# Performance work log

Hardware: AMD Instinct MI355X
Metric: run time of the kernel (lower is better)

## Reference

```python
import jax, jax.numpy as jnp
import numpy as np

N, E, G = 10000, 160000, 64          # nodes, edges, graphs
T, FIN, ED, FOUT = 5, 75, 50, 15     # towers, channels, edge-emb dim, per-tower out
EPS_BN, EPS_STD = 1e-5, 1e-5


def setup_inputs() -> dict:
    key = jax.random.key(0)
    ks = jax.random.split(key, 16)
    s = 0.05
    return dict(
        x=jax.random.randint(ks[0], (N,), 0, 21),
        edge_index=jax.random.randint(ks[1], (2, E), 0, N),
        edge_attr=jax.random.randint(ks[2], (E,), 0, 4),
        batch=jnp.sort(jax.random.randint(ks[3], (N,), 0, G)),
        node_emb=jax.random.normal(ks[4], (21, FIN), dtype=jnp.float32),
        edge_emb=jax.random.normal(ks[5], (4, ED), dtype=jnp.float32),
        We=jax.random.normal(ks[6], (4, ED, FIN), dtype=jnp.float32) * s,
        be=jnp.zeros((4, FIN), jnp.float32),
        Wpre=jax.random.normal(ks[7], (4, T, 3 * FIN, FIN), dtype=jnp.float32) * s,
        bpre=jnp.zeros((4, T, FIN), jnp.float32),
        Wpost=jax.random.normal(ks[8], (4, T, 13 * FIN, FOUT), dtype=jnp.float32) * s,
        bpost=jnp.zeros((4, T, FOUT), jnp.float32),
        Wlin=jax.random.normal(ks[9], (4, FIN, FIN), dtype=jnp.float32) * s,
        blin=jnp.zeros((4, FIN), jnp.float32),
        bn_gamma=jnp.ones((4, FIN), jnp.float32),
        bn_beta=jnp.zeros((4, FIN), jnp.float32),
        uaf=jnp.array([1.1, -0.01, 1e-5, -0.9, 1e-5], dtype=jnp.float32),
        mW1=jax.random.normal(ks[10], (FIN, 50), dtype=jnp.float32) * s,
        mb1=jnp.zeros((50,), jnp.float32),
        mW2=jax.random.normal(ks[11], (50, 25), dtype=jnp.float32) * s,
        mb2=jnp.zeros((25,), jnp.float32),
        mW3=jax.random.normal(ks[12], (25, 1), dtype=jnp.float32) * s,
        mb3=jnp.zeros((1,), jnp.float32),
    )


def _uaf(v, p):
    # softplus(A*(x+B) + C*x^2) - softplus(D*(x-B)) + E
    return (jax.nn.softplus(p[0] * (v + p[1]) + p[2] * v * v)
            - jax.nn.softplus(p[3] * (v - p[1])) + p[4])


def _pna_layer(h, src, dst, e_feat, We, be, Wpre, bpre, Wpost, bpost, Wl, bl,
               deg, avg_log):
    eemb = e_feat @ We + be                      # [E, FIN] edge encoder
    x_i, x_j = h[dst], h[src]                    # [E, FIN] gathers
    # pre-MLP: per-tower Linear(cat[x_i, x_j, e], 3F -> F), split weight blocks
    W1, W2, W3 = Wpre[:, :FIN], Wpre[:, FIN:2 * FIN], Wpre[:, 2 * FIN:]
    m = (jnp.einsum('ec,tcf->etf', x_i, W1)
         + jnp.einsum('ec,tcf->etf', x_j, W2)
         + jnp.einsum('ec,tcf->etf', eemb, W3) + bpre)   # [E, T, FIN]
    degc = jnp.maximum(deg, 1.0)[:, None, None]
    mean = jax.ops.segment_sum(m, dst, N) / degc          # [N, T, FIN]
    mean_sq = jax.ops.segment_sum(m * m, dst, N) / degc
    empty = (deg == 0.0)[:, None, None]
    mn = jnp.where(empty, 0.0, jax.ops.segment_min(m, dst, N))
    mx = jnp.where(empty, 0.0, jax.ops.segment_max(m, dst, N))
    std = jnp.sqrt(jax.nn.relu(mean_sq - mean * mean) + EPS_STD)
    agg = jnp.concatenate([mean, mn, mx, std], axis=-1)   # [N, T, 4F]
    amp = (jnp.log(jnp.maximum(deg, 1.0) + 1.0) / avg_log)[:, None, None]
    out = jnp.concatenate([agg, agg * amp, agg / amp], axis=-1)  # [N, T, 12F]
    # cat tower input (divide_input=False -> full x per tower)
    out = jnp.concatenate(
        [jnp.broadcast_to(h[:, None, :], (N, T, FIN)), out], axis=-1)  # [N,T,13F]
    out = jnp.einsum('ntc,tcf->ntf', out, Wpost) + bpost  # [N, T, FOUT]
    return out.reshape(N, T * FOUT) @ Wl + bl             # [N, FIN]


def reference(node_emb, edge_emb, We, be, Wpre, bpre, Wpost, bpost, Wlin, blin,
              bn_gamma, bn_beta, uaf, mW1, mb1, mW2, mb2, mW3, mb3,
              x, edge_index, edge_attr, batch):
    src, dst = edge_index[0], edge_index[1]
    h = node_emb[x]                              # [N, 75]
    e_feat = edge_emb[edge_attr]                 # [E, 50]
    deg = jax.ops.segment_sum(jnp.ones((E,), h.dtype), dst, N)
    avg_log = jnp.mean(jnp.log(deg + 1.0))       # PNA avg degree (log) statistic
    for l in range(4):
        out = _pna_layer(h, src, dst, e_feat, We[l], be[l], Wpre[l], bpre[l],
                         Wpost[l], bpost[l], Wlin[l], blin[l], deg, avg_log)
        mu = out.mean(axis=0)
        var = out.var(axis=0)                    # biased, training-mode BN
        out = (out - mu) * jax.lax.rsqrt(var + EPS_BN) * bn_gamma[l] + bn_beta[l]
        h = _uaf(out, uaf)
    pooled = jax.ops.segment_sum(h, batch, G)    # global_add_pool -> [G, 75]
    z = _uaf(pooled @ mW1 + mb1, uaf)
    z = _uaf(z @ mW2 + mb2, uaf)
    return z @ mW3 + mb3                         # [G, 1]
```

## Files before the change

### kernel.cpp

```cpp
#include <hip/hip_runtime.h>
#include <hip/hip_fp16.h>
#include <math.h>

static constexpr int N_   = 10000;
static constexpr int E_   = 160000;
static constexpr int G_   = 64;
static constexpr int T_   = 5;
static constexpr int FIN_ = 75;
static constexpr int ED_  = 50;
static constexpr int FOUT_= 15;
static constexpr int TF_  = T_*FIN_;
static constexpr int AGGW_= 4*FIN_;
static constexpr int YC_  = 48;
static constexpr int NP_  = 10112;
static constexpr int AW_  = 400;
static constexpr int BW_  = 384;
static constexpr int WK_  = 380;

__device__ __forceinline__ float softplus_f(float x){
    return fmaxf(x, 0.f) + log1pf(expf(-fabsf(x)));
}
__device__ __forceinline__ float uaf_f(float v, const float* __restrict__ p){
    return softplus_f(p[0]*(v + p[1]) + p[2]*v*v) - softplus_f(p[3]*(v - p[1])) + p[4];
}
__device__ __forceinline__ unsigned pack2h(float a, float b){
    __half2 h = __floats2half2_rn(a, b);
    return *reinterpret_cast<unsigned*>(&h);
}

__global__ void k_h0(const int* __restrict__ x, const float* __restrict__ node_emb, float* __restrict__ hT){
    int i = blockIdx.x*blockDim.x + threadIdx.x;
    if (i >= 80*N_) return;
    int q = i / N_, n = i % N_;
    hT[(size_t)q*NP_ + n] = (q < FIN_) ? node_emb[x[n]*FIN_ + q] : 0.f;
}

__global__ void k_deg(const int* __restrict__ ei, int* __restrict__ deg_i){
    int e = blockIdx.x*blockDim.x + threadIdx.x;
    if (e >= E_) return;
    atomicAdd(&deg_i[ei[E_ + e]], 1);
}

__global__ void k_scan(const int* __restrict__ deg_i, int* __restrict__ offs, float* __restrict__ avglog){
    __shared__ int sd[1024];
    __shared__ float sf[1024];
    __shared__ int carry;
    if (threadIdx.x == 0) carry = 0;
    __syncthreads();
    float ls = 0.f;
    for (int base = 0; base < N_; base += 1024){
        int i = base + threadIdx.x;
        int v = (i < N_) ? deg_i[i] : 0;
        if (i < N_) ls += logf((float)v + 1.f);
        sd[threadIdx.x] = v;
        __syncthreads();
        for (int off = 1; off < 1024; off <<= 1){
            int t = (threadIdx.x >= off) ? sd[threadIdx.x - off] : 0;
            __syncthreads();
            sd[threadIdx.x] += t;
            __syncthreads();
        }
        if (i < N_) offs[i] = carry + sd[threadIdx.x] - v;
        __syncthreads();
        if (threadIdx.x == 0) carry += sd[1023];
        __syncthreads();
    }
    if (threadIdx.x == 0) offs[N_] = carry;
    sf[threadIdx.x] = ls;
    __syncthreads();
    for (int off = 512; off > 0; off >>= 1){
        if (threadIdx.x < off) sf[threadIdx.x] += sf[threadIdx.x + off];
        __syncthreads();
    }
    if (threadIdx.x == 0) avglog[0] = sf[0] / (float)N_;
}

__global__ void k_fill(const int* __restrict__ ei, const int* __restrict__ eattr,
                       const int* __restrict__ offs, int* __restrict__ cursor, int* __restrict__ csr){
    int e = blockIdx.x*blockDim.x + threadIdx.x;
    if (e >= E_) return;
    int d = ei[E_ + e];
    int pos = offs[d] + atomicAdd(&cursor[d], 1);
    csr[pos] = ei[e] | (eattr[e] << 16);
}

__global__ void k_amp(const int* __restrict__ deg_i, const float* __restrict__ avglog,
                      float* __restrict__ ampv, float* __restrict__ iampv){
    int n = blockIdx.x*blockDim.x + threadIdx.x;
    if (n >= N_) return;
    float dm = fmaxf((float)deg_i[n], 1.f);
    float a = logf(dm + 1.f) / avglog[0];
    ampv[n] = a;
    iampv[n] = 1.f / a;
}

__global__ void k_eemb(const float* __restrict__ edge_emb, const float* __restrict__ We,
                       const float* __restrict__ be, float* __restrict__ eembw){
    int i = blockIdx.x*blockDim.x + threadIdx.x;
    if (i >= 4*4*FIN_) return;
    int c = i % FIN_;
    int a = (i / FIN_) % 4;
    int l = i / (4*FIN_);
    float s = be[l*FIN_ + c];
    for (int k = 0; k < ED_; k++) s = fmaf(edge_emb[a*ED_ + k], We[(l*ED_ + k)*FIN_ + c], s);
    eembw[i] = s;
}

__global__ void k_tbl(const float* __restrict__ eembw, const float* __restrict__ Wpre,
                      const float* __restrict__ bpre, float* __restrict__ tbl){
    int i = blockIdx.x*blockDim.x + threadIdx.x;
    if (i >= 4*4*TF_) return;
    int f = i % FIN_;
    int t = (i / FIN_) % T_;
    int a = (i / TF_) % 4;
    int l = i / (4*TF_);
    float s = bpre[(l*T_ + t)*FIN_ + f];
    const float* em = eembw + (l*4 + a)*FIN_;
    const float* W3 = Wpre + ((size_t)(l*T_ + t)*225 + 2*FIN_)*FIN_;
    for (int c = 0; c < FIN_; c++) s = fmaf(em[c], W3[c*FIN_ + f], s);
    tbl[i] = s;
}

__global__ void k_wcomb(const float* __restrict__ Wpost, float* __restrict__ Wcomb){
    int i = blockIdx.x*blockDim.x + threadIdx.x;
    if (i >= 4*T_*WK_*YC_) return;
    int j = i % YC_;
    int c = (i / YC_) % WK_;
    int t = (i / (YC_*WK_)) % T_;
    int l = i / (YC_*WK_*T_);
    float v = 0.f;
    if (j < 45){
        int blk = j / 15, fo = j % 15;
        const float* Wp = Wpost + (size_t)(l*T_ + t)*975*15;
        if (c < FIN_){ if (blk == 0) v = Wp[c*15 + fo]; }
        else if (c >= 80){
            int r = c - 80;
            int fi = r >> 2, kind = r & 3;
            v = Wp[(FIN_ + blk*AGGW_ + kind*FIN_ + fi)*15 + fo];
        }
    }
    Wcomb[i] = v;
}

__global__ void k_wlin80(const float* __restrict__ Wlin, float* __restrict__ Wlin80){
    int i = blockIdx.x*blockDim.x + threadIdx.x;
    if (i >= 4*FIN_*80) return;
    int q = i % 80;
    int p = (i / 80) % FIN_;
    int l = i / (80*FIN_);
    Wlin80[i] = (q < FIN_) ? Wlin[(l*FIN_ + p)*FIN_ + q] : 0.f;
}

__global__ void __launch_bounds__(256) k_A3(const float* __restrict__ hT, const float* __restrict__ Wpre_l,
                                            float* __restrict__ Af, __half* __restrict__ Bh){
    __shared__ float smem[15600];
    float* Wt   = smem;
    float* ActS = smem + 6000;
    float* Out  = smem;
    int chunk = blockIdx.y;
    int t = chunk >> 1, half = chunk & 1;
    const float* __restrict__ W = Wpre_l + (size_t)(t*225 + half*FIN_)*FIN_;
    int n0 = blockIdx.x * 128;
    int tid = threadIdx.x;
    for (int i = tid; i < FIN_*80; i += 256){
        int r = i / 80, c = i - r*80;
        Wt[i] = (c < FIN_) ? W[r*FIN_ + c] : 0.f;
    }
    for (int i = tid; i < FIN_*128; i += 256){
        int r = i >> 7, n = i & 127;
        ActS[i] = hT[(size_t)r*NP_ + n0 + n];
    }
    __syncthreads();
    int tn = tid & 31, tj = tid >> 5;
    float acc[4][10];
    #pragma unroll
    for (int m = 0; m < 4; m++)
        #pragma unroll
        for (int j = 0; j < 10; j++) acc[m][j] = 0.f;
    #pragma unroll 5
    for (int k = 0; k < FIN_; k++){
        float4 av = *(const float4*)(ActS + (k<<7) + (tn<<2));
        const float* wr = Wt + k*80 + tj*10;
        #pragma unroll
        for (int j = 0; j < 10; j++){
            float wv = wr[j];
            acc[0][j] = fmaf(av.x, wv, acc[0][j]);
            acc[1][j] = fmaf(av.y, wv, acc[1][j]);
            acc[2][j] = fmaf(av.z, wv, acc[2][j]);
            acc[3][j] = fmaf(av.w, wv, acc[3][j]);
        }
    }
    __syncthreads();
    #pragma unroll
    for (int m = 0; m < 4; m++)
        #pragma unroll
        for (int j = 0; j < 10; j++)
            Out[(tn*4 + m)*81 + tj*10 + j] = acc[m][j];
    __syncthreads();
    if (half == 0){
        for (int i = tid; i < 128*20; i += 256){
            int node = i / 20, q4 = i % 20;
            int gn = n0 + node;
            if (gn < N_){
                const float* src = Out + node*81 + q4*4;
                *(float4*)(Af + (size_t)gn*AW_ + t*80 + q4*4) = make_float4(src[0], src[1], src[2], src[3]);
            }
        }
    } else {
        for (int i = tid; i < 128*38; i += 256){
            int node = i / 38, q = i % 38;
            int gn = n0 + node;
            if (gn < N_){
                const float* src = Out + node*81 + 2*q;
                *(unsigned*)((__half*)Bh + (size_t)gn*BW_ + t*76 + 2*q) = pack2h(src[0], src[1]);
            }
        }
    }
}

__global__ void __launch_bounds__(128) k_agg(const float* __restrict__ Af, const __half* __restrict__ Bh,
                                             const int* __restrict__ offs, const int* __restrict__ csr,
                                             const float* __restrict__ tbl_l, uint2* __restrict__ agg2h){
    __shared__ float tl[4*TF_];
    int bid = blockIdx.x;
    int n = (bid & 7)*1250 + (bid >> 3);
    for (int idx = threadIdx.x; idx < 4*TF_; idx += 128) tl[idx] = tbl_l[idx];
    __syncthreads();
    int s = offs[n], e_end = offs[n+1];
    int f0 = threadIdx.x;
    int f1 = threadIdx.x + 128;
    int f2r = threadIdx.x + 256;
    int f2 = (f2r < TF_) ? f2r : 0;
    int aoA0 = (f0/FIN_)*80 + f0%FIN_;
    int aoA1 = (f1/FIN_)*80 + f1%FIN_;
    int aoA2 = (f2/FIN_)*80 + f2%FIN_;
    int aoB0 = (f0/FIN_)*76 + f0%FIN_;
    int aoB1 = (f1/FIN_)*76 + f1%FIN_;
    int aoB2 = (f2/FIN_)*76 + f2%FIN_;
    const float* An = Af + (size_t)n*AW_;
    float a0 = An[aoA0], a1 = An[aoA1], a2 = An[aoA2];
    float s0=0.f,s1=0.f,s2=0.f, q0=0.f,q1=0.f,q2=0.f;
    float mn0=INFINITY,mn1=INFINITY,mn2=INFINITY;
    float mx0=-INFINITY,mx1=-INFINITY,mx2=-INFINITY;
    int e = s;
    for (; e + 3 < e_end; e += 4){
        float b0[4], b1[4], b2[4];
        const float* tt[4];
        #pragma unroll
        for (int u = 0; u < 4; u++){
            int pk = csr[e + u];
            const __half* B = Bh + (size_t)(pk & 0xFFFF)*BW_;
            tt[u] = tl + (pk >> 16)*TF_;
            b0[u] = __half2float(B[aoB0]);
            b1[u] = __half2float(B[aoB1]);
            b2[u] = __half2float(B[aoB2]);
        }
        #pragma unroll
        for (int u = 0; u < 4; u++){
            float m0 = a0 + b0[u] + tt[u][f0];
            float m1 = a1 + b1[u] + tt[u][f1];
            float m2 = a2 + b2[u] + tt[u][f2];
            s0 += m0; s1 += m1; s2 += m2;
            q0 = fmaf(m0,m0,q0); q1 = fmaf(m1,m1,q1); q2 = fmaf(m2,m2,q2);
            mn0 = fminf(mn0,m0); mx0 = fmaxf(mx0,m0);
            mn1 = fminf(mn1,m1); mx1 = fmaxf(mx1,m1);
            mn2 = fminf(mn2,m2); mx2 = fmaxf(mx2,m2);
        }
    }
    for (; e < e_end; e++){
        int pk = csr[e];
        const __half* B = Bh + (size_t)(pk & 0xFFFF)*BW_;
        const float* t0 = tl + (pk >> 16)*TF_;
        float m0 = a0 + __half2float(B[aoB0]) + t0[f0];
        float m1 = a1 + __half2float(B[aoB1]) + t0[f1];
        float m2 = a2 + __half2float(B[aoB2]) + t0[f2];
        s0 += m0; q0 = fmaf(m0,m0,q0); mn0 = fminf(mn0,m0); mx0 = fmaxf(mx0,m0);
        s1 += m1; q1 = fmaf(m1,m1,q1); mn1 = fminf(mn1,m1); mx1 = fmaxf(mx1,m1);
        s2 += m2; q2 = fmaf(m2,m2,q2); mn2 = fminf(mn2,m2); mx2 = fmaxf(mx2,m2);
    }
    float deg = (float)(e_end - s);
    float dc = fmaxf(deg, 1.f);
    float inv = 1.f / dc;
    bool empty = (deg == 0.f);
    {
        float mean = s0*inv;
        float sd = sqrtf(fmaxf(q0*inv - mean*mean, 0.f) + 1e-5f);
        int t = f0/FIN_, fi = f0%FIN_;
        uint2 o; o.x = pack2h(mean, empty?0.f:mn0); o.y = pack2h(empty?0.f:mx0, sd);
        agg2h[(size_t)(t*FIN_+fi)*NP_ + n] = o;
    }
    {
        float mean = s1*inv;
        float sd = sqrtf(fmaxf(q1*inv - mean*mean, 0.f) + 1e-5f);
        int t = f1/FIN_, fi = f1%FIN_;
        uint2 o; o.x = pack2h(mean, empty?0.f:mn1); o.y = pack2h(empty?0.f:mx1, sd);
        agg2h[(size_t)(t*FIN_+fi)*NP_ + n] = o;
    }
    if (f2r < TF_){
        float mean = s2*inv;
        float sd = sqrtf(fmaxf(q2*inv - mean*mean, 0.f) + 1e-5f);
        int t = f2r/FIN_, fi = f2r%FIN_;
        uint2 o; o.x = pack2h(mean, empty?0.f:mn2); o.y = pack2h(empty?0.f:mx2, sd);
        agg2h[(size_t)(t*FIN_+fi)*NP_ + n] = o;
    }
}

__device__ __forceinline__ void unp4_64(float* Ad, int i, uint2 u){
    int fq = i >> 6, n = i & 63;
    __half2 lo = *reinterpret_cast<__half2*>(&u.x);
    __half2 hi = *reinterpret_cast<__half2*>(&u.y);
    Ad[(fq*4+0)*64 + n] = __low2float(lo);
    Ad[(fq*4+1)*64 + n] = __high2float(lo);
    Ad[(fq*4+2)*64 + n] = __low2float(hi);
    Ad[(fq*4+3)*64 + n] = __high2float(hi);
}

__global__ void __launch_bounds__(128) k_post6(const float* __restrict__ hT, const uint2* __restrict__ agg2h,
                                               const float* __restrict__ Wcomb_l,
                                               float* __restrict__ Yp0, float* __restrict__ Yp1){
    __shared__ float Act[2][20*64];
    __shared__ float Wt[2][20*YC_];
    int t = blockIdx.y;
    int kz = blockIdx.z;
    int c0 = kz ? 9 : 0;
    int c1 = kz ? 19 : 9;
    float* __restrict__ Yp = kz ? Yp1 : Yp0;
    int n0 = blockIdx.x * 64;
    int tid = threadIdx.x;
    int tn = tid & 15, tj = tid >> 4;
    const float* __restrict__ Wl = Wcomb_l + (size_t)t*WK_*YC_;
    const uint2* __restrict__ agt = agg2h + (size_t)t*FIN_*NP_;

    if (c0 < 4){
        const float* sp = hT + (size_t)(c0*20)*NP_ + n0;
        for (int i = tid; i < 320; i += 128){
            int r = i >> 4, c4 = i & 15;
            *(float4*)(&Act[0][r*64 + c4*4]) = *(const float4*)(sp + (size_t)r*NP_ + c4*4);
        }
    } else {
        const uint2* sp = agt + (size_t)((c0 - 4)*5)*NP_ + n0;
        for (int i = tid; i < 320; i += 128)
            unp4_64(Act[0], i, sp[(size_t)(i >> 6)*NP_ + (i & 63)]);
    }
    for (int i = tid; i < 240; i += 128){
        int r = i / 12, c4 = i % 12;
        *(float4*)(&Wt[0][r*YC_ + c4*4]) = *(const float4*)(Wl + (size_t)(c0*20 + r)*YC_ + c4*4);
    }
    __syncthreads();

    float acc[4][6];
    #pragma unroll
    for (int m = 0; m < 4; m++)
        #pragma unroll
        for (int j = 0; j < 6; j++) acc[m][j] = 0.f;

    float4 ph0, ph1, ph2, pw0, pw1;
    uint2  pb0, pb1, pb2;
    #pragma unroll 1
    for (int ch = c0; ch < c1; ch++){
        int buf = (ch - c0) & 1;
        int ch1 = ch + 1;
        bool have = (ch1 < c1);
        bool nh = (ch1 < 4);
        if (have){
            if (nh){
                const float* sp = hT + (size_t)(ch1*20)*NP_ + n0;
                { int i0 = tid;       ph0 = *(const float4*)(sp + (size_t)(i0 >> 4)*NP_ + (i0 & 15)*4); }
                { int i1 = tid + 128; ph1 = *(const float4*)(sp + (size_t)(i1 >> 4)*NP_ + (i1 & 15)*4); }
                if (tid < 64){ int i2 = tid + 256; ph2 = *(const float4*)(sp + (size_t)(i2 >> 4)*NP_ + (i2 & 15)*4); }
            } else {
                const uint2* sp = agt + (size_t)((ch1 - 4)*5)*NP_ + n0;
                { int i0 = tid;       pb0 = sp[(size_t)(i0 >> 6)*NP_ + (i0 & 63)]; }
                { int i1 = tid + 128; pb1 = sp[(size_t)(i1 >> 6)*NP_ + (i1 & 63)]; }
                if (tid < 64){ int i2 = tid + 256; pb2 = sp[(size_t)(i2 >> 6)*NP_ + (i2 & 63)]; }
            }
            { int i = tid; int r = i / 12, c4 = i % 12;
              pw0 = *(const float4*)(Wl + (size_t)(ch1*20 + r)*YC_ + c4*4); }
            if (tid < 112){ int i = tid + 128; int r = i / 12, c4 = i % 12;
              pw1 = *(const float4*)(Wl + (size_t)(ch1*20 + r)*YC_ + c4*4); }
        }
        const float* A = Act[buf];
        const float* Wb = Wt[buf];
        #pragma unroll
        for (int k = 0; k < 20; k++){
            float4 av = *(const float4*)(A + (k<<6) + (tn<<2));
            const float* wr = Wb + k*YC_ + tj*6;
            #pragma unroll
            for (int j = 0; j < 6; j++){
                float wv = wr[j];
                acc[0][j] = fmaf(av.x, wv, acc[0][j]);
                acc[1][j] = fmaf(av.y, wv, acc[1][j]);
                acc[2][j] = fmaf(av.z, wv, acc[2][j]);
                acc[3][j] = fmaf(av.w, wv, acc[3][j]);
            }
        }
        if (have){
            float* Ad = Act[buf ^ 1];
            float* Wd = Wt[buf ^ 1];
            if (nh){
                { int i0 = tid;       *(float4*)(&Ad[(i0 >> 4)*64 + (i0 & 15)*4]) = ph0; }
                { int i1 = tid + 128; *(float4*)(&Ad[(i1 >> 4)*64 + (i1 & 15)*4]) = ph1; }
                if (tid < 64){ int i2 = tid + 256; *(float4*)(&Ad[(i2 >> 4)*64 + (i2 & 15)*4]) = ph2; }
            } else {
                unp4_64(Ad, tid, pb0);
                unp4_64(Ad, tid + 128, pb1);
                if (tid < 64) unp4_64(Ad, tid + 256, pb2);
            }
            { int i = tid; int r = i / 12, c4 = i % 12; *(float4*)(&Wd[r*YC_ + c4*4]) = pw0; }
            if (tid < 112){ int i = tid + 128; int r = i / 12, c4 = i % 12; *(float4*)(&Wd[r*YC_ + c4*4]) = pw1; }
            __syncthreads();
        }
    }
    int nodeb = n0 + tn*4;
    #pragma unroll
    for (int j = 0; j < 6; j++){
        int col = t*YC_ + tj*6 + j;
        float4 v = make_float4(acc[0][j], acc[1][j], acc[2][j], acc[3][j]);
        if (nodeb + 3 < N_){
            *(float4*)(Yp + (size_t)col*NP_ + nodeb) = v;
        } else {
            #pragma unroll
            for (int m = 0; m < 4; m++)
                if (nodeb + m < N_) Yp[(size_t)col*NP_ + nodeb + m] = (&v.x)[m];
        }
    }
}

__global__ void __launch_bounds__(64) k_Y(const float* __restrict__ Yp0, const float* __restrict__ Yp1,
                                          const float* __restrict__ ampv,
                                          const float* __restrict__ iampv, const float* __restrict__ bpost_l,
                                          const float* __restrict__ Wlin80_l, const float* __restrict__ blin_l,
                                          float* __restrict__ olinT, float* __restrict__ bnsum, float* __restrict__ bnsq){
    __shared__ float st[64*77];
    int qbase = blockIdx.y * 40;
    int qcnt  = blockIdx.y ? 35 : 40;
    int n = blockIdx.x*64 + threadIdx.x;
    int nn = (n < N_) ? n : N_-1;
    bool valid = (n < N_);
    float amp = ampv[nn], iamp = iampv[nn];
    #pragma unroll 1
    for (int t = 0; t < T_; t++){
        #pragma unroll
        for (int fo = 0; fo < FOUT_; fo++){
            size_t b0 = (size_t)(t*YC_ + fo)*NP_ + nn;
            size_t b1 = (size_t)(t*YC_ + 15 + fo)*NP_ + nn;
            size_t b2 = (size_t)(t*YC_ + 30 + fo)*NP_ + nn;
            float v = (Yp0[b0] + Yp1[b0])
                    + amp  * (Yp0[b1] + Yp1[b1])
                    + iamp * (Yp0[b2] + Yp1[b2])
                    + bpost_l[t*FOUT_ + fo];
            st[threadIdx.x*77 + t*FOUT_ + fo] = v;
        }
    }
    __syncthreads();
    float acc[40];
    #pragma unroll
    for (int k = 0; k < 40; k++) acc[k] = (qbase + k < FIN_) ? blin_l[qbase + k] : 0.f;
    #pragma unroll 1
    for (int p = 0; p < FIN_; p++){
        float yv = st[threadIdx.x*77 + p];
        const float* Wp = Wlin80_l + p*80 + qbase;
        #pragma unroll
        for (int k = 0; k < 40; k++) acc[k] = fmaf(yv, Wp[k], acc[k]);
    }
    if (valid){
        #pragma unroll
        for (int k = 0; k < 40; k++){
            int q = qbase + k;
            if (q < FIN_) olinT[(size_t)q*NP_ + n] = acc[k];
        }
    }
    __syncthreads();
    #pragma unroll
    for (int k = 0; k < 40; k++) st[threadIdx.x*77 + k] = valid ? acc[k] : 0.f;
    __syncthreads();
    for (int qq = threadIdx.x; qq < qcnt; qq += 64){
        float s = 0.f, s2 = 0.f;
        #pragma unroll 4
        for (int m = 0; m < 64; m++){ float v = st[m*77 + qq]; s += v; s2 = fmaf(v, v, s2); }
        atomicAdd(&bnsum[qbase + qq], s);
        atomicAdd(&bnsq[qbase + qq], s2);
    }
}

__global__ void k_bn(const float* __restrict__ olinT, const float* __restrict__ bnsum, const float* __restrict__ bnsq,
                     const float* __restrict__ gamma_l, const float* __restrict__ beta_l,
                     const float* __restrict__ uafp, float* __restrict__ hT){
    int i = blockIdx.x*blockDim.x + threadIdx.x;
    if (i >= FIN_*N_) return;
    int q = i / N_, n = i % N_;
    float mu = bnsum[q] * (1.f/(float)N_);
    float var = bnsq[q] * (1.f/(float)N_) - mu*mu;
    float xh = (olinT[(size_t)q*NP_ + n] - mu) * rsqrtf(var + 1e-5f) * gamma_l[q] + beta_l[q];
    hT[(size_t)q*NP_ + n] = uaf_f(xh, uafp);
}

__global__ void __launch_bounds__(256) k_pool2(const float* __restrict__ hT, const int* __restrict__ batch,
                                               float* __restrict__ pooled){
    __shared__ int sb[2];
    int g = blockIdx.x;
    if (threadIdx.x < 2){
        int key = g + threadIdx.x;
        int lo = 0, hi = N_;
        while (lo < hi){ int mid = (lo + hi) >> 1; if (batch[mid] < key) lo = mid + 1; else hi = mid; }
        sb[threadIdx.x] = lo;
    }
    __syncthreads();
    int s = sb[0], e = sb[1];
    int wave = threadIdx.x >> 6, lane = threadIdx.x & 63;
    for (int q = wave; q < FIN_; q += 4){
        float sum = 0.f;
        for (int n = s + lane; n < e; n += 64) sum += hT[(size_t)q*NP_ + n];
        #pragma unroll
        for (int off = 32; off > 0; off >>= 1) sum += __shfl_down(sum, off);
        if (lane == 0) pooled[g*FIN_ + q] = sum;
    }
}

__global__ void __launch_bounds__(64) k_mlp(const float* __restrict__ pooled,
        const float* __restrict__ mW1, const float* __restrict__ mb1,
        const float* __restrict__ mW2, const float* __restrict__ mb2,
        const float* __restrict__ mW3, const float* __restrict__ mb3,
        const float* __restrict__ uafp, float* __restrict__ outp){
    __shared__ float pr[FIN_];
    __shared__ float z1[50];
    __shared__ float z2[25];
    int g = blockIdx.x;
    for (int c = threadIdx.x; c < FIN_; c += 64) pr[c] = pooled[g*FIN_ + c];
    __syncthreads();
    if (threadIdx.x < 50){
        float s = mb1[threadIdx.x];
        for (int c = 0; c < FIN_; c++) s = fmaf(pr[c], mW1[c*50 + threadIdx.x], s);
        z1[threadIdx.x] = uaf_f(s, uafp);
    }
    __syncthreads();
    if (threadIdx.x < 25){
        float s = mb2[threadIdx.x];
        for (int c = 0; c < 50; c++) s = fmaf(z1[c], mW2[c*25 + threadIdx.x], s);
        z2[threadIdx.x] = uaf_f(s, uafp);
    }
    __syncthreads();
    if (threadIdx.x == 0){
        float s = mb3[0];
        for (int c = 0; c < 25; c++) s = fmaf(z2[c], mW3[c], s);
        outp[g] = s;
    }
}

extern "C" void kernel_launch(void* const* d_in, const int* in_sizes, int n_in,
                              void* d_out, int out_size, void* d_ws, size_t ws_size,
                              hipStream_t stream) {
    const int* x         = (const int*)d_in[0];
    const int* ei        = (const int*)d_in[1];
    const int* eattr     = (const int*)d_in[2];
    const int* batch     = (const int*)d_in[3];
    const float* node_emb= (const float*)d_in[4];
    const float* edge_emb= (const float*)d_in[5];
    const float* We      = (const float*)d_in[6];
    const float* be      = (const float*)d_in[7];
    const float* Wpre    = (const float*)d_in[8];
    const float* bpre    = (const float*)d_in[9];
    const float* Wpost   = (const float*)d_in[10];
    const float* bpost   = (const float*)d_in[11];
    const float* Wlin    = (const float*)d_in[12];
    const float* blin    = (const float*)d_in[13];
    const float* bn_gamma= (const float*)d_in[14];
    const float* bn_beta = (const float*)d_in[15];
    const float* uafp    = (const float*)d_in[16];
    const float* mW1     = (const float*)d_in[17];
    const float* mb1     = (const float*)d_in[18];
    const float* mW2     = (const float*)d_in[19];
    const float* mb2     = (const float*)d_in[20];
    const float* mW3     = (const float*)d_in[21];
    const float* mb3     = (const float*)d_in[22];
    float* outp          = (float*)d_out;

    char* w = (char*)d_ws;
    auto alloc = [&](size_t bytes) -> void* {
        void* p = (void*)w;
        w += (bytes + 255) & ~(size_t)255;
        return p;
    };
    float*  hT    = (float*)alloc((size_t)80*NP_*4);
    float*  Af    = (float*)alloc((size_t)N_*AW_*4);
    __half* Bh    = (__half*)alloc((size_t)N_*BW_*2);
    uint2*  agg2h = (uint2*)alloc((size_t)TF_*NP_*8);
    float*  Yp0   = (float*)alloc((size_t)T_*YC_*NP_*4);
    float*  Yp1   = (float*)alloc((size_t)T_*YC_*NP_*4);
    float*  olinT = (float*)alloc((size_t)FIN_*NP_*4);
    float*  ampv  = (float*)alloc(N_*4);
    float*  iampv = (float*)alloc(N_*4);
    float*  avglog= (float*)alloc(4);
    float*  tbl   = (float*)alloc(4*4*TF_*4);
    float*  eembw = (float*)alloc(4*4*FIN_*4);
    float*  Wcomb = (float*)alloc((size_t)4*T_*WK_*YC_*4);
    float*  Wlin80= (float*)alloc(4*FIN_*80*4);
    float*  bnsum = (float*)alloc(2*FIN_*4);
    float*  bnsq  = bnsum + FIN_;
    float*  pooled= (float*)alloc(G_*FIN_*4);
    int* deg_i   = (int*)alloc(N_*4);
    int* offs    = (int*)alloc((N_+1)*4);
    int* cursor  = (int*)alloc(N_*4);
    int* csr     = (int*)alloc(E_*4);

    hipMemsetAsync(deg_i, 0, N_*4, stream);
    hipMemsetAsync(cursor, 0, N_*4, stream);

    k_h0<<<(80*N_ + 255)/256, 256, 0, stream>>>(x, node_emb, hT);
    k_deg<<<(E_ + 255)/256, 256, 0, stream>>>(ei, deg_i);
    k_scan<<<1, 1024, 0, stream>>>(deg_i, offs, avglog);
    k_fill<<<(E_ + 255)/256, 256, 0, stream>>>(ei, eattr, offs, cursor, csr);
    k_amp<<<(N_ + 255)/256, 256, 0, stream>>>(deg_i, avglog, ampv, iampv);
    k_eemb<<<(4*4*FIN_ + 255)/256, 256, 0, stream>>>(edge_emb, We, be, eembw);
    k_tbl<<<(4*4*TF_ + 255)/256, 256, 0, stream>>>(eembw, Wpre, bpre, tbl);
    k_wcomb<<<(4*T_*WK_*YC_ + 255)/256, 256, 0, stream>>>(Wpost, Wcomb);
    k_wlin80<<<(4*FIN_*80 + 255)/256, 256, 0, stream>>>(Wlin, Wlin80);

    int nmb = (N_ + 127)/128;
    int npb = (N_ + 63)/64;
    for (int l = 0; l < 4; l++){
        hipMemsetAsync(bnsum, 0, 2*FIN_*4, stream);
        k_A3<<<dim3(nmb, 10), 256, 0, stream>>>(hT, Wpre + (size_t)l*T_*225*FIN_, Af, Bh);
        k_agg<<<N_, 128, 0, stream>>>(Af, Bh, offs, csr, tbl + (size_t)l*4*TF_, agg2h);
        k_post6<<<dim3(npb, T_, 2), 128, 0, stream>>>(hT, agg2h, Wcomb + (size_t)l*T_*WK_*YC_, Yp0, Yp1);
        k_Y<<<dim3(npb, 2), 64, 0, stream>>>(Yp0, Yp1, ampv, iampv, bpost + l*T_*FOUT_,
                                             Wlin80 + (size_t)l*FIN_*80, blin + l*FIN_,
                                             olinT, bnsum, bnsq);
        k_bn<<<(FIN_*N_ + 255)/256, 256, 0, stream>>>(olinT, bnsum, bnsq,
                                                      bn_gamma + l*FIN_, bn_beta + l*FIN_, uafp, hT);
    }

    k_pool2<<<G_, 256, 0, stream>>>(hT, batch, pooled);
    k_mlp<<<G_, 64, 0, stream>>>(pooled, mW1, mb1, mW2, mb2, mW3, mb3, uafp, outp);
}
```

Baseline: 860.7 us.

## Double-buffer K-chunks in pre-MLP GEMM with padded pre-packed weights and smaller tiles

Replaces the pre-MLP node-projection kernel with a version that uses 64-node tiles and 128 threads. It streams the K dimension in four 20-row chunks through double-buffered shared memory, holding the next chunk's loads in registers while the current chunk computes. Weights are pre-padded once into an 80x80 layout so tiles can be loaded with float4 reads. The goal is lower shared-memory use, higher occupancy and latency hiding for global loads, at the cost of extra barriers and more registers.

```diff
diff --git a/kernel.cpp b/kernel.cpp
--- a/kernel.cpp
+++ b/kernel.cpp
@@ -142,6 +142,20 @@
     Wcomb[i] = v;
 }
 
+__global__ void k_wpre80(const float* __restrict__ Wpre, float* __restrict__ Wpre80){
+    int i = blockIdx.x*blockDim.x + threadIdx.x;
+    if (i >= 4*10*80*80) return;
+    int c = i % 80;
+    int r = (i / 80) % 80;
+    int chunk = (i / 6400) % 10;
+    int l = i / 64000;
+    int t = chunk >> 1, half = chunk & 1;
+    float v = 0.f;
+    if (r < FIN_ && c < FIN_)
+        v = Wpre[((size_t)(l*T_ + t)*225 + half*FIN_ + r)*FIN_ + c];
+    Wpre80[i] = v;
+}
+
 __global__ void k_wlin80(const float* __restrict__ Wlin, float* __restrict__ Wlin80){
     int i = blockIdx.x*blockDim.x + threadIdx.x;
     if (i >= 4*FIN_*80) return;
@@ -151,46 +165,82 @@
     Wlin80[i] = (q < FIN_) ? Wlin[(l*FIN_ + p)*FIN_ + q] : 0.f;
 }
 
-__global__ void __launch_bounds__(256) k_A3(const float* __restrict__ hT, const float* __restrict__ Wpre_l,
+__global__ void __launch_bounds__(128) k_A4(const float* __restrict__ hT, const float* __restrict__ Wpre80_l,
                                             float* __restrict__ Af, __half* __restrict__ Bh){
-    __shared__ float smem[15600];
-    float* Wt   = smem;
-    float* ActS = smem + 6000;
-    float* Out  = smem;
-    int chunk = blockIdx.y;
-    int t = chunk >> 1, half = chunk & 1;
-    const float* __restrict__ W = Wpre_l + (size_t)(t*225 + half*FIN_)*FIN_;
-    int n0 = blockIdx.x * 128;
+    __shared__ float smem[5760];
+    float* ActB = smem;
+    float* WtB  = smem + 2560;
+    int chunkid = blockIdx.y;
+    int t = chunkid >> 1, half = chunkid & 1;
+    const float* __restrict__ Wl = Wpre80_l + (size_t)chunkid*6400;
+    int n0 = blockIdx.x * 64;
     int tid = threadIdx.x;
-    for (int i = tid; i < FIN_*80; i += 256){
-        int r = i / 80, c = i - r*80;
-        Wt[i] = (c < FIN_) ? W[r*FIN_ + c] : 0.f;
-    }
-    for (int i = tid; i < FIN_*128; i += 256){
-        int r = i >> 7, n = i & 127;
-        ActS[i] = hT[(size_t)r*NP_ + n0 + n];
-    }
-    __syncthreads();
-    int tn = tid & 31, tj = tid >> 5;
+    int tn = tid & 15, tj = tid >> 4;
+
+    for (int i = tid; i < 320; i += 128){
+        int r = i >> 4, c4 = i & 15;
+        *(float4*)(&ActB[r*64 + c4*4]) = *(const float4*)(hT + (size_t)r*NP_ + n0 + c4*4);
+    }
+    for (int i = tid; i < 400; i += 128){
+        int r = i / 20, c4 = i % 20;
+        *(float4*)(&WtB[r*80 + c4*4]) = *(const float4*)(Wl + r*80 + c4*4);
+    }
+    __syncthreads();
+
     float acc[4][10];
     #pragma unroll
     for (int m = 0; m < 4; m++)
         #pragma unroll
         for (int j = 0; j < 10; j++) acc[m][j] = 0.f;
-    #pragma unroll 5
-    for (int k = 0; k < FIN_; k++){
-        float4 av = *(const float4*)(ActS + (k<<7) + (tn<<2));
-        const float* wr = Wt + k*80 + tj*10;
-        #pragma unroll
-        for (int j = 0; j < 10; j++){
-            float wv = wr[j];
-            acc[0][j] = fmaf(av.x, wv, acc[0][j]);
-            acc[1][j] = fmaf(av.y, wv, acc[1][j]);
-            acc[2][j] = fmaf(av.z, wv, acc[2][j]);
-            acc[3][j] = fmaf(av.w, wv, acc[3][j]);
-        }
-    }
-    __syncthreads();
+
+    float4 ph0, ph1, ph2, pw0, pw1, pw2, pw3;
+    #pragma unroll 1
+    for (int ch = 0; ch < 4; ch++){
+        int buf = ch & 1;
+        bool have = (ch + 1 < 4);
+        if (have){
+            const float* sp = hT + (size_t)((ch+1)*20)*NP_ + n0;
+            { int i0 = tid;       ph0 = *(const float4*)(sp + (size_t)(i0 >> 4)*NP_ + (i0 & 15)*4); }
+            { int i1 = tid + 128; ph1 = *(const float4*)(sp + (size_t)(i1 >> 4)*NP_ + (i1 & 15)*4); }
+            if (tid < 64){ int i2 = tid + 256; ph2 = *(const float4*)(sp + (size_t)(i2 >> 4)*NP_ + (i2 & 15)*4); }
+            const float* wp = Wl + (ch+1)*1600;
+            { int i = tid;       pw0 = *(const float4*)(wp + (i/20)*80 + (i%20)*4); }
+            { int i = tid + 128; pw1 = *(const float4*)(wp + (i/20)*80 + (i%20)*4); }
+            { int i = tid + 256; pw2 = *(const float4*)(wp + (i/20)*80 + (i%20)*4); }
+            if (tid < 16){ int i = tid + 384; pw3 = *(const float4*)(wp + (i/20)*80 + (i%20)*4); }
+        }
+        const float* A  = ActB + buf*1280;
+        const float* Wb = WtB + buf*1600;
+        #pragma unroll
+        for (int k = 0; k < 20; k++){
+            float4 av = *(const float4*)(A + (k<<6) + (tn<<2));
+            const float2* wr = (const float2*)(Wb + k*80 + tj*10);
+            float wv[10];
+            #pragma unroll
+            for (int j2 = 0; j2 < 5; j2++){ float2 w2 = wr[j2]; wv[2*j2] = w2.x; wv[2*j2+1] = w2.y; }
+            #pragma unroll
+            for (int j = 0; j < 10; j++){
+                acc[0][j] = fmaf(av.x, wv[j], acc[0][j]);
+                acc[1][j] = fmaf(av.y, wv[j], acc[1][j]);
+                acc[2][j] = fmaf(av.z, wv[j], acc[2][j]);
+                acc[3][j] = fmaf(av.w, wv[j], acc[3][j]);
+            }
+        }
+        if (have){
+            float* Ad = ActB + (buf ^ 1)*1280;
+            float* Wd = WtB + (buf ^ 1)*1600;
+            { int i0 = tid;       *(float4*)(&Ad[(i0 >> 4)*64 + (i0 & 15)*4]) = ph0; }
+            { int i1 = tid + 128; *(float4*)(&Ad[(i1 >> 4)*64 + (i1 & 15)*4]) = ph1; }
+            if (tid < 64){ int i2 = tid + 256; *(float4*)(&Ad[(i2 >> 4)*64 + (i2 & 15)*4]) = ph2; }
+            { int i = tid;       *(float4*)(&Wd[(i/20)*80 + (i%20)*4]) = pw0; }
+            { int i = tid + 128; *(float4*)(&Wd[(i/20)*80 + (i%20)*4]) = pw1; }
+            { int i = tid + 256; *(float4*)(&Wd[(i/20)*80 + (i%20)*4]) = pw2; }
+            if (tid < 16){ int i = tid + 384; *(float4*)(&Wd[(i/20)*80 + (i%20)*4]) = pw3; }
+            __syncthreads();
+        }
+    }
+    __syncthreads();
+    float* Out = smem;
     #pragma unroll
     for (int m = 0; m < 4; m++)
         #pragma unroll
@@ -198,7 +248,7 @@
             Out[(tn*4 + m)*81 + tj*10 + j] = acc[m][j];
     __syncthreads();
     if (half == 0){
-        for (int i = tid; i < 128*20; i += 256){
+        for (int i = tid; i < 64*20; i += 128){
             int node = i / 20, q4 = i % 20;
             int gn = n0 + node;
             if (gn < N_){
@@ -207,7 +257,7 @@
             }
         }
     } else {
-        for (int i = tid; i < 128*38; i += 256){
+        for (int i = tid; i < 64*38; i += 128){
             int node = i / 38, q = i % 38;
             int gn = n0 + node;
             if (gn < N_){
@@ -594,6 +644,7 @@
     float*  tbl   = (float*)alloc(4*4*TF_*4);
     float*  eembw = (float*)alloc(4*4*FIN_*4);
     float*  Wcomb = (float*)alloc((size_t)4*T_*WK_*YC_*4);
+    float*  Wpre80= (float*)alloc((size_t)4*10*80*80*4);
     float*  Wlin80= (float*)alloc(4*FIN_*80*4);
     float*  bnsum = (float*)alloc(2*FIN_*4);
     float*  bnsq  = bnsum + FIN_;
@@ -614,13 +665,14 @@
     k_eemb<<<(4*4*FIN_ + 255)/256, 256, 0, stream>>>(edge_emb, We, be, eembw);
     k_tbl<<<(4*4*TF_ + 255)/256, 256, 0, stream>>>(eembw, Wpre, bpre, tbl);
     k_wcomb<<<(4*T_*WK_*YC_ + 255)/256, 256, 0, stream>>>(Wpost, Wcomb);
+    k_wpre80<<<(4*10*80*80 + 255)/256, 256, 0, stream>>>(Wpre, Wpre80);
     k_wlin80<<<(4*FIN_*80 + 255)/256, 256, 0, stream>>>(Wlin, Wlin80);
 
-    int nmb = (N_ + 127)/128;
+    int nab = NP_/64;
     int npb = (N_ + 63)/64;
     for (int l = 0; l < 4; l++){
         hipMemsetAsync(bnsum, 0, 2*FIN_*4, stream);
-        k_A3<<<dim3(nmb, 10), 256, 0, stream>>>(hT, Wpre + (size_t)l*T_*225*FIN_, Af, Bh);
+        k_A4<<<dim3(nab, 10), 128, 0, stream>>>(hT, Wpre80 + (size_t)l*10*6400, Af, Bh);
         k_agg<<<N_, 128, 0, stream>>>(Af, Bh, offs, csr, tbl + (size_t)l*4*TF_, agg2h);
         k_post6<<<dim3(npb, T_, 2), 128, 0, stream>>>(hT, agg2h, Wcomb + (size_t)l*T_*WK_*YC_, Yp0, Yp1);
         k_Y<<<dim3(npb, 2), 64, 0, stream>>>(Yp0, Yp1, ampv, iampv, bpost + l*T_*FOUT_,
```

After: 875.9 us. Within noise of the previous version (+1.8%).
